# Performance work log

Measured on AMD Instinct MI355X. Metric: run time of the kernel, lower is better.

Reference implementation:

```python
import jax, jax.numpy as jnp
import numpy as np
import math

B, S, D, H = 2, 2048, 1024, 16
DH = D // H

def setup_inputs() -> dict:
    key0 = jax.random.key(0)
    ks = jax.random.split(key0, 12)
    s = 1.0 / math.sqrt(D)
    return {
        "query": jax.random.normal(ks[0], (B, S, D), jnp.float32),
        "key": jax.random.normal(ks[1], (B, S, D), jnp.float32),
        "value": jax.random.normal(ks[2], (B, S, D), jnp.float32),
        "mask": jax.random.randint(ks[3], (B, 1, S, S), 0, 2, jnp.int32),
        "Wq": jax.random.normal(ks[4], (D, D), jnp.float32) * s,
        "bq": jnp.zeros((D,), jnp.float32),
        "Wk": jax.random.normal(ks[5], (D, D), jnp.float32) * s,
        "bk": jnp.zeros((D,), jnp.float32),
        "Wv": jax.random.normal(ks[6], (D, D), jnp.float32) * s,
        "bv": jnp.zeros((D,), jnp.float32),
        "Wo": jax.random.normal(ks[7], (D, D), jnp.float32) * s,
        "bo": jnp.zeros((D,), jnp.float32),
    }

def reference(query, key, value, mask, Wq, bq, Wk, bk, Wv, bv, Wo, bo):
    # Linear projections (torch Linear: x @ W.T + b)
    q = query @ Wq.T + bq
    k = key @ Wk.T + bk
    v = value @ Wv.T + bv
    # [B, S, D] -> [B, H, S, DH]
    q = q.reshape(B, S, H, DH).transpose(0, 2, 1, 3)
    k = k.reshape(B, S, H, DH).transpose(0, 2, 1, 3)
    v = v.reshape(B, S, H, DH).transpose(0, 2, 1, 3)
    # scaled dot-product attention with explicit [B,H,S,S] scores
    score = jnp.einsum('bhqd,bhkd->bhqk', q, k) / math.sqrt(DH)
    score = jnp.where(mask == 0, jnp.float32(-1e9), score)
    attn = jax.nn.softmax(score, axis=-1)
    out = jnp.einsum('bhqk,bhkd->bhqd', attn, v)
    out = out.transpose(0, 2, 1, 3).reshape(B, S, D)
    return out @ Wo.T + bo
```

## Files before the change

kernel.cpp:

```cpp
#include <hip/hip_runtime.h>
#include <hip/hip_bf16.h>

typedef __attribute__((ext_vector_type(4))) float f32x4;
typedef __attribute__((ext_vector_type(8))) short bf16x8;
typedef __attribute__((ext_vector_type(4))) short s16x4;
typedef __attribute__((ext_vector_type(4))) unsigned int u32x4;
typedef unsigned short ushort_t;
typedef unsigned int u32;
typedef unsigned long long u64;

constexpr int B = 2, S = 2048, D = 1024, H = 16, DH = 64;

__device__ __forceinline__ ushort_t f2bf(float f) {
    union { float f; unsigned int i; } v; v.f = f;
    unsigned int r = v.i + 0x7fffu + ((v.i >> 16) & 1u);
    return (ushort_t)(r >> 16);
}

__device__ __forceinline__ float fast_exp2(float x) {
#if __has_builtin(__builtin_amdgcn_exp2f)
    return __builtin_amdgcn_exp2f(x);
#else
    return exp2f(x);
#endif
}

__device__ __forceinline__ u32 pack_hi16(u32 b1, u32 b0) {
#if __has_builtin(__builtin_amdgcn_perm)
    return __builtin_amdgcn_perm(b1, b0, 0x07060302u);
#else
    return (b1 & 0xffff0000u) | (b0 >> 16);
#endif
}

__device__ __forceinline__ void gload_lds16(const void* g, void* l) {
    __builtin_amdgcn_global_load_lds(
        (const __attribute__((address_space(1))) unsigned int*)g,
        (__attribute__((address_space(3))) unsigned int*)l,
        16, 0, 0);
}

__global__ __launch_bounds__(256) void cvt_f32_bf16(
    const float* __restrict__ in, ushort_t* __restrict__ out, int n)
{
    int i = (blockIdx.x * 256 + threadIdx.x) * 4;
    if (i >= n) return;
    f32x4 v = *(const f32x4*)(in + i);
    s16x4 o;
    for (int j = 0; j < 4; ++j) o[j] = (short)f2bf(v[j]);
    *(s16x4*)(out + i) = o;
}

__global__ __launch_bounds__(256) void cvt3_f32_bf16(
    const float* __restrict__ a0, const float* __restrict__ a1,
    const float* __restrict__ a2, ushort_t* __restrict__ out, int n)
{
    const float* in = blockIdx.y == 0 ? a0 : (blockIdx.y == 1 ? a1 : a2);
    int i = (blockIdx.x * 256 + threadIdx.x) * 4;
    if (i >= n) return;
    f32x4 v = *(const f32x4*)(in + i);
    s16x4 o;
    for (int j = 0; j < 4; ++j) o[j] = (short)f2bf(v[j]);
    *(s16x4*)(out + (size_t)blockIdx.y * n + i) = o;
}

__global__ __launch_bounds__(256) void cvt4_f32_bf16(
    const float* __restrict__ a0, const float* __restrict__ a1,
    const float* __restrict__ a2, const float* __restrict__ a3,
    ushort_t* __restrict__ out, int n)
{
    const float* in = blockIdx.y == 0 ? a0 : (blockIdx.y == 1 ? a1 :
                      (blockIdx.y == 2 ? a2 : a3));
    int i = (blockIdx.x * 256 + threadIdx.x) * 4;
    if (i >= n) return;
    f32x4 v = *(const f32x4*)(in + i);
    s16x4 o;
    for (int j = 0; j < 4; ++j) o[j] = (short)f2bf(v[j]);
    *(s16x4*)(out + (size_t)blockIdx.y * n + i) = o;
}

__global__ __launch_bounds__(256) void pack_mask(
    const int* __restrict__ mask, u64* __restrict__ pm)
{
    const int wave_g = (blockIdx.x * 256 + threadIdx.x) >> 6;
    const int lane = threadIdx.x & 63;
    for (int w = 0; w < 16; ++w) {
        size_t idx = (size_t)wave_g * 16 + w;
        int mv = mask[idx * 64 + lane];
        u64 bal = __ballot(mv != 0);
        if (lane == 0) {
            int t = (int)(idx & 31);
            int q = (int)((idx >> 5) & (S - 1));
            int b = (int)(idx >> 16);
            pm[((size_t)b * 32 + t) * S + q] = bal;
        }
    }
}

__global__ __launch_bounds__(256) void transpose_v(
    const ushort_t* __restrict__ Vw, ushort_t* __restrict__ Vt)
{
    __shared__ ushort_t T[64][80];
    const int st = blockIdx.x, bh = blockIdx.y;
    const int b = bh / H, h = bh % H;
    const int tid = threadIdx.x;
    const int r = tid >> 3, c = tid & 7;
    for (int p = 0; p < 2; ++p) {
        int s = p * 32 + r;
        bf16x8 v = *(const bf16x8*)(Vw + (size_t)(b * S + st * 64 + s) * D + h * DH + c * 8);
        *(bf16x8*)(&T[s][c * 8]) = v;
    }
    __syncthreads();
    const int q0q = (c >> 2) * 8 + (c & 3);
    for (int p = 0; p < 2; ++p) {
        int d = p * 32 + r;
        bf16x8 o;
        for (int j = 0; j < 4; ++j) o[j]     = (short)T[q0q * 4 + j][d];
        for (int j = 0; j < 4; ++j) o[4 + j] = (short)T[(q0q + 4) * 4 + j][d];
        *(bf16x8*)(Vt + (size_t)((b * H + h) * DH + d) * S + st * 64 + c * 8) = o;
    }
}

template <typename OutT>
__device__ __forceinline__ void gemm_body128(
    const ushort_t* __restrict__ Ag,
    const ushort_t* __restrict__ Wg,
    const float* __restrict__ bias,
    OutT* __restrict__ Cg,
    ushort_t* __restrict__ VtOut,
    int M, int N, int K,
    ushort_t* As, ushort_t* Bs, bool vepi)
{
    constexpr int BK = 64;
    const int tid  = threadIdx.x;
    const int wid  = tid >> 6;
    const int lane = tid & 63;
    const int m0 = blockIdx.x * 128;
    const int n0 = blockIdx.y * 128;
    const int wr = wid >> 1, wc = wid & 1;

    const int lrow = lane & 15;
    const int lk8  = (lane >> 4) * 8;
    const int srow  = lane >> 3;
    const int sbyte = (lane & 7) * 16;

    f32x4 acc[4][4] = {};

    for (int k0 = 0; k0 < K; k0 += BK) {
        #pragma unroll
        for (int c = 0; c < 4; ++c) {
            int r0 = wid * 32 + c * 8;
            gload_lds16((const char*)(Ag + (size_t)(m0 + r0 + srow) * K + k0) + sbyte,
                        (char*)As + r0 * 128);
            gload_lds16((const char*)(Wg + (size_t)(n0 + r0 + srow) * K + k0) + sbyte,
                        (char*)Bs + r0 * 128);
        }
        __syncthreads();

        #pragma unroll
        for (int kk = 0; kk < BK; kk += 32) {
            bf16x8 af[4], bfr[4];
            #pragma unroll
            for (int i = 0; i < 4; ++i) {
                af[i]  = *(const bf16x8*)(As + (wr * 64 + i * 16 + lrow) * BK + kk + lk8);
                bfr[i] = *(const bf16x8*)(Bs + (wc * 64 + i * 16 + lrow) * BK + kk + lk8);
            }
            #pragma unroll
            for (int i = 0; i < 4; ++i)
                #pragma unroll
                for (int j = 0; j < 4; ++j)
                    acc[i][j] = __builtin_amdgcn_mfma_f32_16x16x32_bf16(
                        af[i], bfr[j], acc[i][j], 0, 0, 0);
        }
        __syncthreads();
    }

    const int hi    = lane >> 4;
    const int crow0 = hi * 4;
    const int ccol  = lane & 15;

    if (vepi) {
        #pragma unroll
        for (int j = 0; j < 4; ++j) {
            int col = n0 + wc * 64 + j * 16 + ccol;
            float bv = bias[col];
            int hv = col >> 6, d = col & 63;
            #pragma unroll
            for (int i = 0; i < 4; ++i) {
                int row = m0 + wr * 64 + i * 16 + crow0;
                int b = row >> 11;
                int s = row & (S - 1);
                int sbase = s & ~63;
                int pos = ((i >> 1) * 4 + hi) * 8 + (i & 1) * 4;
                s16x4 o;
                #pragma unroll
                for (int r = 0; r < 4; ++r) o[r] = (short)f2bf(acc[i][j][r] + bv);
                *(s16x4*)(VtOut + ((size_t)(b * H + hv) * DH + d) * S + sbase + pos) = o;
            }
        }
    } else {
        #pragma unroll
        for (int j = 0; j < 4; ++j) {
            int col = n0 + wc * 64 + j * 16 + ccol;
            float bv = bias[col];
            #pragma unroll
            for (int i = 0; i < 4; ++i) {
                #pragma unroll
                for (int r = 0; r < 4; ++r) {
                    int row = m0 + wr * 64 + i * 16 + crow0 + r;
                    float val = acc[i][j][r] + bv;
                    if constexpr (__is_same(OutT, float))
                        Cg[(size_t)row * N + col] = val;
                    else
                        Cg[(size_t)row * N + col] = f2bf(val);
                }
            }
        }
    }
}

template <typename OutT>
__device__ __forceinline__ void gemm_body64(
    const ushort_t* __restrict__ Ag,
    const ushort_t* __restrict__ Wg,
    const float* __restrict__ bias,
    OutT* __restrict__ Cg,
    int M, int N, int K,
    ushort_t* As, ushort_t* Bs)
{
    constexpr int BK = 64;
    const int tid  = threadIdx.x;
    const int wid  = tid >> 6;
    const int lane = tid & 63;
    const int m0 = blockIdx.x * 128;
    const int n0 = blockIdx.y * 64;
    const int wr = wid >> 1, wc = wid & 1;

    const int lrow = lane & 15;
    const int lk8  = (lane >> 4) * 8;
    const int srow  = lane >> 3;
    const int sbyte = (lane & 7) * 16;

    f32x4 acc[4][2] = {};

    for (int k0 = 0; k0 < K; k0 += BK) {
        #pragma unroll
        for (int c = 0; c < 4; ++c) {
            int r0 = wid * 32 + c * 8;
            gload_lds16((const char*)(Ag + (size_t)(m0 + r0 + srow) * K + k0) + sbyte,
                        (char*)As + r0 * 128);
        }
        #pragma unroll
        for (int c = 0; c < 2; ++c) {
            int r0 = wid * 16 + c * 8;
            gload_lds16((const char*)(Wg + (size_t)(n0 + r0 + srow) * K + k0) + sbyte,
                        (char*)Bs + r0 * 128);
        }
        __syncthreads();

        #pragma unroll
        for (int kk = 0; kk < BK; kk += 32) {
            bf16x8 af[4], bfr[2];
            #pragma unroll
            for (int i = 0; i < 4; ++i)
                af[i]  = *(const bf16x8*)(As + (wr * 64 + i * 16 + lrow) * BK + kk + lk8);
            #pragma unroll
            for (int j = 0; j < 2; ++j)
                bfr[j] = *(const bf16x8*)(Bs + (wc * 32 + j * 16 + lrow) * BK + kk + lk8);
            #pragma unroll
            for (int i = 0; i < 4; ++i)
                #pragma unroll
                for (int j = 0; j < 2; ++j)
                    acc[i][j] = __builtin_amdgcn_mfma_f32_16x16x32_bf16(
                        af[i], bfr[j], acc[i][j], 0, 0, 0);
        }
        __syncthreads();
    }

    const int crow0 = (lane >> 4) * 4;
    const int ccol  = lane & 15;
    #pragma unroll
    for (int j = 0; j < 2; ++j) {
        int col = n0 + wc * 32 + j * 16 + ccol;
        float bv = bias[col];
        #pragma unroll
        for (int i = 0; i < 4; ++i) {
            #pragma unroll
            for (int r = 0; r < 4; ++r) {
                int row = m0 + wr * 64 + i * 16 + crow0 + r;
                float val = acc[i][j][r] + bv;
                if constexpr (__is_same(OutT, float))
                    Cg[(size_t)row * N + col] = val;
                else
                    Cg[(size_t)row * N + col] = f2bf(val);
            }
        }
    }
}

template <typename OutT>
__global__ __launch_bounds__(256, 4) void gemm_bt_bias(
    const ushort_t* __restrict__ Ag, const ushort_t* __restrict__ Wg,
    const float* __restrict__ bias, OutT* __restrict__ Cg,
    int M, int N, int K)
{
    __shared__ ushort_t As[128 * 64];
    __shared__ ushort_t Bs[64 * 64];
    gemm_body64<OutT>(Ag, Wg, bias, Cg, M, N, K, As, Bs);
}

__global__ __launch_bounds__(256, 2) void gemm_qkv(
    const ushort_t* __restrict__ X3,
    const ushort_t* __restrict__ W4,
    const float* __restrict__ b0, const float* __restrict__ b1,
    const float* __restrict__ b2,
    ushort_t* __restrict__ QKV,
    ushort_t* __restrict__ Vt,
    int M, int N, int K)
{
    __shared__ ushort_t As[128 * 64];
    __shared__ ushort_t Bs[128 * 64];
    const int z = blockIdx.z;
    const float* bias = z == 0 ? b0 : (z == 1 ? b1 : b2);
    gemm_body128<ushort_t>(X3 + (size_t)z * M * K, W4 + (size_t)z * N * K,
                           bias, QKV + (size_t)z * M * N, Vt,
                           M, N, K, As, Bs, z == 2);
}

__global__ __launch_bounds__(256, 4) void attn_kernel(
    const ushort_t* __restrict__ Q,
    const ushort_t* __restrict__ Kt,
    const ushort_t* __restrict__ Vt,
    const u64* __restrict__ pmask,
    ushort_t* __restrict__ O)
{
    constexpr int KVBLK = 64;
    constexpr int NT = S / KVBLK;
    constexpr float C1 = 0.18033688f;
    constexpr float C2 = 17.31234049f;
    __shared__ ushort_t Ks[KVBLK * DH];
    __shared__ ushort_t Vs[KVBLK * DH];

    const int tid  = threadIdx.x;
    const int wid  = tid >> 6;
    const int lane = tid & 63;
    const int qt = blockIdx.x;
    const int bh = blockIdx.y;
    const int b = bh / H, h = bh % H;
    const int q0 = qt * 64 + wid * 16;

    const int lq   = lane & 15;
    const int hi   = lane >> 4;
    const int lk8  = hi * 8;
    const int srow = lane >> 3;
    const int sbyte = (((lane & 7) ^ srow) & 7) * 16;

    bf16x8 qf[2];
    #pragma unroll
    for (int kk = 0; kk < 2; ++kk)
        qf[kk] = *(const bf16x8*)(Q + (size_t)(b * S + q0 + lq) * D + h * DH + kk * 32 + lk8);

    f32x4 oacc[4] = {};
    f32x4 ps = {};
    const u32x4 onesw = {0x3f803f80u, 0x3f803f80u, 0x3f803f80u, 0x3f803f80u};
    const bf16x8 onesf = __builtin_bit_cast(bf16x8, onesw);

    const u64* pmrow = pmask + (size_t)b * 32 * S + q0 + lq;
    const ushort_t* Vtb = Vt + (size_t)(b * H + h) * DH * S;

    for (int t = 0; t < NT; ++t) {
        const int kv0 = t * KVBLK;
        #pragma unroll
        for (int c = 0; c < 2; ++c) {
            int r0 = wid * 16 + c * 8;
            gload_lds16((const char*)(Kt + (size_t)(b * S + kv0 + r0 + srow) * D + h * DH) + sbyte,
                        (char*)Ks + r0 * 128);
            gload_lds16((const char*)(Vtb + (size_t)(r0 + srow) * S + kv0) + sbyte,
                        (char*)Vs + r0 * 128);
        }
        const u64 mw = pmrow[(size_t)t * S];
        __syncthreads();

        f32x4 sc[4] = {};
        #pragma unroll
        for (int kk = 0; kk < 2; ++kk) {
            const int chunk = ((kk * 4 + hi) ^ (lq & 7)) * 8;
            #pragma unroll
            for (int ni = 0; ni < 4; ++ni) {
                bf16x8 kf = *(const bf16x8*)(Ks + (ni * 16 + lq) * 64 + chunk);
                sc[ni] = __builtin_amdgcn_mfma_f32_16x16x32_bf16(kf, qf[kk], sc[ni], 0, 0, 0);
            }
        }

        const u32 lo32 = (u32)mw;
        const u32 hi32 = (u32)(mw >> 32);
        u32 paw[8];
        #pragma unroll
        for (int ni = 0; ni < 4; ++ni) {
            const u32 word = (ni < 2) ? lo32 : hi32;
            const int base = (ni & 1) * 16 + hi * 4;
            u32 pb[4];
            #pragma unroll
            for (int r = 0; r < 4; ++r) {
                float p = fast_exp2(__builtin_fmaf(sc[ni][r], C1, -C2));
                int mbit = ((int)(word << (31 - (base + r)))) >> 31;
                pb[r] = __builtin_bit_cast(u32, p) & (u32)mbit;
            }
            paw[ni * 2]     = pack_hi16(pb[1], pb[0]);
            paw[ni * 2 + 1] = pack_hi16(pb[3], pb[2]);
        }

        #pragma unroll
        for (int kk = 0; kk < 2; ++kk) {
            u32x4 pv = {paw[kk * 4], paw[kk * 4 + 1], paw[kk * 4 + 2], paw[kk * 4 + 3]};
            bf16x8 paf = __builtin_bit_cast(bf16x8, pv);
            ps = __builtin_amdgcn_mfma_f32_16x16x32_bf16(paf, onesf, ps, 0, 0, 0);
            const int chunk = ((kk * 4 + hi) ^ (lq & 7)) * 8;
            #pragma unroll
            for (int di = 0; di < 4; ++di) {
                bf16x8 vf = *(const bf16x8*)(Vs + (di * 16 + lq) * 64 + chunk);
                oacc[di] = __builtin_amdgcn_mfma_f32_16x16x32_bf16(paf, vf, oacc[di], 0, 0, 0);
            }
        }
        __syncthreads();
    }

    float inv[4];
    #pragma unroll
    for (int r = 0; r < 4; ++r) inv[r] = 1.0f / ps[r];
    #pragma unroll
    for (int di = 0; di < 4; ++di) {
        #pragma unroll
        for (int r = 0; r < 4; ++r) {
            float v = oacc[di][r] * inv[r];
            O[(size_t)(b * S + q0 + hi * 4 + r) * D + h * DH + di * 16 + lq] = f2bf(v);
        }
    }
}

extern "C" void kernel_launch(void* const* d_in, const int* in_sizes, int n_in,
                              void* d_out, int out_size, void* d_ws, size_t ws_size,
                              hipStream_t stream) {
    const float* query = (const float*)d_in[0];
    const float* key   = (const float*)d_in[1];
    const float* value = (const float*)d_in[2];
    const int*   mask  = (const int*)d_in[3];
    const float* Wq = (const float*)d_in[4];
    const float* bq = (const float*)d_in[5];
    const float* Wk = (const float*)d_in[6];
    const float* bk = (const float*)d_in[7];
    const float* Wv = (const float*)d_in[8];
    const float* bv = (const float*)d_in[9];
    const float* Wo = (const float*)d_in[10];
    const float* bo = (const float*)d_in[11];
    float* out = (float*)d_out;

    const int M = B * S;
    const int NX = M * D;
    const int NW = D * D;

    char* ws = (char*)d_ws;
    const size_t MB = 1024 * 1024;
    dim3 gblk64(M / 128, D / 64);
    const int gcX = NX / (4 * 256);
    const int gcW = NW / (4 * 256);
    const int pmBlocks = (B * S * (S / 64)) / (16 * 4);

    if (ws_size >= 58 * MB) {
        ushort_t* X3  = (ushort_t*)(ws);
        ushort_t* Ow  = (ushort_t*)(ws + 8 * MB);
        ushort_t* W4  = (ushort_t*)(ws + 24 * MB);
        ushort_t* QKV = (ushort_t*)(ws + 32 * MB);
        ushort_t* Qw = QKV, *Kw = QKV + NX;
        ushort_t* Vtb = QKV + 2 * (size_t)NX;
        u64* pm = (u64*)(ws + 56 * MB);

        cvt3_f32_bf16<<<dim3(gcX, 3), 256, 0, stream>>>(query, key, value, X3, NX);
        cvt4_f32_bf16<<<dim3(gcW, 4), 256, 0, stream>>>(Wq, Wk, Wv, Wo, W4, NW);
        pack_mask<<<pmBlocks, 256, 0, stream>>>(mask, pm);

        gemm_qkv<<<dim3(M / 128, D / 128, 3), 256, 0, stream>>>(
            X3, W4, bq, bk, bv, QKV, Vtb, M, D, D);

        attn_kernel<<<dim3(S / 64, B * H), 256, 0, stream>>>(Qw, Kw, Vtb, pm, Ow);

        gemm_bt_bias<float><<<gblk64, 256, 0, stream>>>(Ow, W4 + 3 * (size_t)NW, bo, out, M, D, D);
    } else {
        ushort_t* Xb = (ushort_t*)(ws);
        ushort_t* Vtb = (ushort_t*)(ws);
        ushort_t* Wb = (ushort_t*)(ws + 8  * MB);
        u64*      pm = (u64*)(ws + 8 * MB);
        ushort_t* Qw = (ushort_t*)(ws + 16 * MB);
        ushort_t* Kw = (ushort_t*)(ws + 24 * MB);
        ushort_t* Vw = (ushort_t*)(ws + 32 * MB);
        ushort_t* Ow = (ushort_t*)(ws + 40 * MB);

        cvt_f32_bf16<<<gcX, 256, 0, stream>>>(query, Xb, NX);
        cvt_f32_bf16<<<gcW, 256, 0, stream>>>(Wq, Wb, NW);
        gemm_bt_bias<ushort_t><<<gblk64, 256, 0, stream>>>(Xb, Wb, bq, Qw, M, D, D);

        cvt_f32_bf16<<<gcX, 256, 0, stream>>>(key, Xb, NX);
        cvt_f32_bf16<<<gcW, 256, 0, stream>>>(Wk, Wb, NW);
        gemm_bt_bias<ushort_t><<<gblk64, 256, 0, stream>>>(Xb, Wb, bk, Kw, M, D, D);

        cvt_f32_bf16<<<gcX, 256, 0, stream>>>(value, Xb, NX);
        cvt_f32_bf16<<<gcW, 256, 0, stream>>>(Wv, Wb, NW);
        gemm_bt_bias<ushort_t><<<gblk64, 256, 0, stream>>>(Xb, Wb, bv, Vw, M, D, D);

        transpose_v<<<dim3(S / 64, B * H), 256, 0, stream>>>(Vw, Vtb);
        pack_mask<<<pmBlocks, 256, 0, stream>>>(mask, pm);

        attn_kernel<<<dim3(S / 64, B * H), 256, 0, stream>>>(Qw, Kw, Vtb, pm, Ow);

        cvt_f32_bf16<<<gcW, 256, 0, stream>>>(Wo, Wb, NW);
        gemm_bt_bias<float><<<gblk64, 256, 0, stream>>>(Ow, Wb, bo, out, M, D, D);
    }
}
```

Baseline: 140.5 us.

## Stage V-transpose epilogue through LDS and process two KV tiles per barrier

```diff
diff --git a/kernel.cpp b/kernel.cpp
--- a/kernel.cpp
+++ b/kernel.cpp
@@ -129,9 +129,11 @@
     OutT* __restrict__ Cg,
     ushort_t* __restrict__ VtOut,
     int M, int N, int K,
-    ushort_t* As, ushort_t* Bs, bool vepi)
+    ushort_t* SH, bool vepi)
 {
     constexpr int BK = 64;
+    ushort_t* As = SH;
+    ushort_t* Bs = SH + 128 * 64;
     const int tid  = threadIdx.x;
     const int wid  = tid >> 6;
     const int lane = tid & 63;
@@ -182,21 +184,27 @@
     if (vepi) {
         #pragma unroll
         for (int j = 0; j < 4; ++j) {
-            int col = n0 + wc * 64 + j * 16 + ccol;
-            float bv = bias[col];
-            int hv = col >> 6, d = col & 63;
+            int dl = wc * 64 + j * 16 + ccol;
+            float bv = bias[n0 + dl];
             #pragma unroll
             for (int i = 0; i < 4; ++i) {
-                int row = m0 + wr * 64 + i * 16 + crow0;
-                int b = row >> 11;
-                int s = row & (S - 1);
-                int sbase = s & ~63;
-                int pos = ((i >> 1) * 4 + hi) * 8 + (i & 1) * 4;
+                int pos = wr * 64 + ((i >> 1) * 4 + hi) * 8 + (i & 1) * 4;
                 s16x4 o;
                 #pragma unroll
                 for (int r = 0; r < 4; ++r) o[r] = (short)f2bf(acc[i][j][r] + bv);
-                *(s16x4*)(VtOut + ((size_t)(b * H + hv) * DH + d) * S + sbase + pos) = o;
-            }
+                *(s16x4*)(SH + dl * 132 + pos) = o;
+            }
+        }
+        __syncthreads();
+        const int b = m0 >> 11;
+        const int sbase = m0 & (S - 1);
+        #pragma unroll
+        for (int rr = 0; rr < 32; ++rr) {
+            int dl = wid * 32 + rr;
+            int dg = n0 + dl;
+            u32 w2 = *(const u32*)(SH + dl * 132 + lane * 2);
+            *(u32*)(VtOut + ((size_t)(b * H + (dg >> 6)) * DH + (dg & 63)) * S
+                    + sbase + lane * 2) = w2;
         }
     } else {
         #pragma unroll
@@ -318,13 +326,12 @@
     ushort_t* __restrict__ Vt,
     int M, int N, int K)
 {
-    __shared__ ushort_t As[128 * 64];
-    __shared__ ushort_t Bs[128 * 64];
+    __shared__ ushort_t SH[128 * 132];
     const int z = blockIdx.z;
     const float* bias = z == 0 ? b0 : (z == 1 ? b1 : b2);
     gemm_body128<ushort_t>(X3 + (size_t)z * M * K, W4 + (size_t)z * N * K,
                            bias, QKV + (size_t)z * M * N, Vt,
-                           M, N, K, As, Bs, z == 2);
+                           M, N, K, SH, z == 2);
 }
 
 __global__ __launch_bounds__(256, 4) void attn_kernel(
@@ -334,12 +341,11 @@
     const u64* __restrict__ pmask,
     ushort_t* __restrict__ O)
 {
-    constexpr int KVBLK = 64;
-    constexpr int NT = S / KVBLK;
+    constexpr int NT2 = S / 128;
     constexpr float C1 = 0.18033688f;
     constexpr float C2 = 17.31234049f;
-    __shared__ ushort_t Ks[KVBLK * DH];
-    __shared__ ushort_t Vs[KVBLK * DH];
+    __shared__ ushort_t Ks[2][64 * DH];
+    __shared__ ushort_t Vs[2][64 * DH];
 
     const int tid  = threadIdx.x;
     const int wid  = tid >> 6;
@@ -368,30 +374,17 @@
     const u64* pmrow = pmask + (size_t)b * 32 * S + q0 + lq;
     const ushort_t* Vtb = Vt + (size_t)(b * H + h) * DH * S;
 
-    for (int t = 0; t < NT; ++t) {
-        const int kv0 = t * KVBLK;
-        #pragma unroll
-        for (int c = 0; c < 2; ++c) {
-            int r0 = wid * 16 + c * 8;
-            gload_lds16((const char*)(Kt + (size_t)(b * S + kv0 + r0 + srow) * D + h * DH) + sbyte,
-                        (char*)Ks + r0 * 128);
-            gload_lds16((const char*)(Vtb + (size_t)(r0 + srow) * S + kv0) + sbyte,
-                        (char*)Vs + r0 * 128);
-        }
-        const u64 mw = pmrow[(size_t)t * S];
-        __syncthreads();
-
+    auto compute = [&](const ushort_t* Kc, const ushort_t* Vc, u64 mw) {
         f32x4 sc[4] = {};
         #pragma unroll
         for (int kk = 0; kk < 2; ++kk) {
             const int chunk = ((kk * 4 + hi) ^ (lq & 7)) * 8;
             #pragma unroll
             for (int ni = 0; ni < 4; ++ni) {
-                bf16x8 kf = *(const bf16x8*)(Ks + (ni * 16 + lq) * 64 + chunk);
+                bf16x8 kf = *(const bf16x8*)(Kc + (ni * 16 + lq) * 64 + chunk);
                 sc[ni] = __builtin_amdgcn_mfma_f32_16x16x32_bf16(kf, qf[kk], sc[ni], 0, 0, 0);
             }
         }
-
         const u32 lo32 = (u32)mw;
         const u32 hi32 = (u32)(mw >> 32);
         u32 paw[8];
@@ -409,7 +402,6 @@
             paw[ni * 2]     = pack_hi16(pb[1], pb[0]);
             paw[ni * 2 + 1] = pack_hi16(pb[3], pb[2]);
         }
-
         #pragma unroll
         for (int kk = 0; kk < 2; ++kk) {
             u32x4 pv = {paw[kk * 4], paw[kk * 4 + 1], paw[kk * 4 + 2], paw[kk * 4 + 3]};
@@ -418,10 +410,31 @@
             const int chunk = ((kk * 4 + hi) ^ (lq & 7)) * 8;
             #pragma unroll
             for (int di = 0; di < 4; ++di) {
-                bf16x8 vf = *(const bf16x8*)(Vs + (di * 16 + lq) * 64 + chunk);
+                bf16x8 vf = *(const bf16x8*)(Vc + (di * 16 + lq) * 64 + chunk);
                 oacc[di] = __builtin_amdgcn_mfma_f32_16x16x32_bf16(paf, vf, oacc[di], 0, 0, 0);
             }
         }
+    };
+
+    for (int t = 0; t < NT2; ++t) {
+        #pragma unroll
+        for (int half = 0; half < 2; ++half) {
+            const int kv0 = (t * 2 + half) * 64;
+            #pragma unroll
+            for (int c = 0; c < 2; ++c) {
+                int r0 = wid * 16 + c * 8;
+                gload_lds16((const char*)(Kt + (size_t)(b * S + kv0 + r0 + srow) * D + h * DH) + sbyte,
+                            (char*)Ks[half] + r0 * 128);
+                gload_lds16((const char*)(Vtb + (size_t)(r0 + srow) * S + kv0) + sbyte,
+                            (char*)Vs[half] + r0 * 128);
+            }
+        }
+        const u64 mwa = pmrow[(size_t)(t * 2) * S];
+        const u64 mwb = pmrow[(size_t)(t * 2 + 1) * S];
+        __syncthreads();
+
+        compute(Ks[0], Vs[0], mwa);
+        compute(Ks[1], Vs[1], mwb);
         __syncthreads();
     }
 
```

Result: no change. 139.5 us (-0.7%).
